# Kernel optimization log

Hardware: AMD Instinct MI355X
Metric: run time of the kernel (lower is better)

Reference implementation:

```python
import jax, jax.numpy as jnp
import numpy as np

ATOM_FDIM = 133
BOND_FDIM = 147
HIDDEN = 300
DEPTH = 3
N_ATOMS = 100000
N_BONDS = 200000
MAX_NB = 6
N_MOLS = 4000


def setup_inputs() -> dict:
    key = jax.random.key(0)
    ks = jax.random.split(key, 10)
    f_atoms = jax.random.normal(ks[0], (N_ATOMS, ATOM_FDIM), dtype=jnp.float32)
    f_bonds = jax.random.normal(ks[1], (N_BONDS, BOND_FDIM), dtype=jnp.float32)
    a2b = jax.random.randint(ks[2], (N_ATOMS, MAX_NB), 0, N_BONDS)
    b2a = jax.random.randint(ks[3], (N_BONDS,), 0, N_ATOMS)
    b2revb = jax.random.randint(ks[4], (N_BONDS,), 0, N_BONDS)
    atom2mol = jnp.sort(jax.random.randint(ks[5], (N_ATOMS,), 0, N_MOLS))
    s = 1.0 / np.sqrt(HIDDEN)
    W_i = jax.random.uniform(ks[6], (BOND_FDIM, HIDDEN), jnp.float32, -s, s)
    W_h = jax.random.uniform(ks[7], (HIDDEN, HIDDEN), jnp.float32, -s, s)
    W_o_w = jax.random.uniform(ks[8], (ATOM_FDIM + HIDDEN, HIDDEN), jnp.float32, -s, s)
    W_o_b = jax.random.uniform(ks[9], (HIDDEN,), jnp.float32, -s, s)
    return {"f_atoms": f_atoms, "f_bonds": f_bonds, "a2b": a2b, "b2a": b2a,
            "b2revb": b2revb, "atom2mol": atom2mol, "W_i": W_i, "W_h": W_h,
            "W_o_w": W_o_w, "W_o_b": W_o_b}


def reference(f_atoms, f_bonds, a2b, b2a, b2revb, atom2mol, W_i, W_h, W_o_w, W_o_b):
    # input = W_i(f_bonds); message = act(input)
    inp = f_bonds @ W_i                      # [n_bonds, hidden]
    message = jax.nn.relu(inp)
    for _ in range(DEPTH - 1):
        # gather neighbor bond messages per atom and sum: [n_atoms, max_nb, h] -> [n_atoms, h]
        a_message = message[a2b].sum(axis=1)
        rev_message = message[b2revb]        # [n_bonds, hidden]
        message = a_message[b2a] - rev_message
        message = jax.nn.relu(inp + message @ W_h)
    # final atom-level aggregation
    a_message = message[a2b].sum(axis=1)     # [n_atoms, hidden]
    a_input = jnp.concatenate([f_atoms, a_message], axis=1)
    atom_hiddens = jax.nn.relu(a_input @ W_o_w + W_o_b)
    # segment mean pooling over molecules
    sums = jax.ops.segment_sum(atom_hiddens, atom2mol, num_segments=N_MOLS)
    counts = jax.ops.segment_sum(jnp.ones((atom_hiddens.shape[0],), atom_hiddens.dtype),
                                 atom2mol, num_segments=N_MOLS)
    mol_vecs = sums / jnp.maximum(counts, 1.0)[:, None]  # zero vec for empty mols
    return mol_vecs
```

## Files before the change

kernel.cpp:

```cpp
#include <hip/hip_runtime.h>
#include <stdint.h>

#define ATOM_FDIM 133
#define BOND_FDIM 147
#define HIDDEN    300
#define N_ATOMS   100000
#define N_BONDS   200000
#define MAX_NB    6
#define N_MOLS    4000

#define KP_I 160
#define KP_H 320
#define KP_O 448
#define LDA  304
#define CPR  38

#define TM   128
#define ACH  8
#define BCH  24

typedef unsigned short u16;
typedef short bf16x8 __attribute__((ext_vector_type(8)));
typedef float f32x4 __attribute__((ext_vector_type(4)));

__device__ __forceinline__ u16 f2bu(float f) {
    unsigned u = __float_as_uint(f);
    u += 0x7FFFu + ((u >> 16) & 1u);
    return (u16)(u >> 16);
}
__device__ __forceinline__ float bu2f(u16 b) { return __uint_as_float(((unsigned)b) << 16); }

__device__ __forceinline__ uint4 relu_bf16x8(uint4 v) {
    union { uint4 u; u16 s[8]; } x, o;
    x.u = v;
    #pragma unroll
    for (int e = 0; e < 8; ++e) o.s[e] = (x.s[e] & 0x8000u) ? (u16)0 : x.s[e];
    return o.u;
}
__device__ __forceinline__ uint4 comb_bf16x8(uint4 vi, uint4 va, uint4 vy) {
    union { uint4 u; u16 s[8]; } xi, xa, xy, o;
    xi.u = vi; xa.u = va; xy.u = vy;
    #pragma unroll
    for (int e = 0; e < 8; ++e)
        o.s[e] = f2bu(fmaxf(bu2f(xi.s[e]) + bu2f(xa.s[e]) - bu2f(xy.s[e]), 0.f));
    return o.u;
}

#define AS1 __attribute__((address_space(1)))
#define AS3 __attribute__((address_space(3)))
__device__ __forceinline__ void gl_lds(const void* g, void* l) {
    __builtin_amdgcn_global_load_lds((const AS1 void*)g, (AS3 void*)l, 16, 0, 0);
}

template <int AM, int EPI>
__global__ __launch_bounds__(512, 2) void mm_k(
    const u16* __restrict__ A, int lda,
    const u16* __restrict__ aYp,
    const u16* __restrict__ Yp,
    const int* __restrict__ b2a,
    const int* __restrict__ b2revb,
    const u16* __restrict__ Wp,
    const float* __restrict__ bias,
    u16* __restrict__ out0, int ldo0,
    int M, int NT)
{
    __shared__ __align__(16) u16 As[3][ACH * 512];
    __shared__ __align__(16) u16 Bs[3][BCH * 512];

    const int t    = threadIdx.x;
    const int lane = t & 63, wid = t >> 6;
    const int fl   = lane & 15, fh = lane >> 4;
    const int m0   = blockIdx.x * TM;
    const int wr   = wid >> 1, wc = wid & 1;

    int arow = m0 + wid * 16 + fl;
    if (arow > M - 1) arow = M - 1;
    const char* srcAp = (const char*)A + (size_t)arow * (size_t)lda * 2u + (size_t)(fh * 16);
    const char* pI = srcAp;
    const char* pA = nullptr; const char* pY = nullptr;
    if constexpr (AM == 2) {
        const int ia = b2a[arow], ir = b2revb[arow];
        pA = (const char*)aYp + (size_t)ia * (LDA * 2) + (size_t)(fh * 16);
        pY = (const char*)Yp  + (size_t)ir * (LDA * 2) + (size_t)(fh * 16);
    }
    const char* WpC = (const char*)Wp;
    const size_t srcB = (size_t)(3 * wid) * 1024u + (size_t)lane * 16u;

    f32x4 acc[2][12] = {};
    uint4 qa0, qa1, qa2, qb0, qb1, qb2;
    (void)qa1; (void)qa2; (void)qb1; (void)qb2;

    if constexpr (AM == 0) {
        gl_lds(srcAp, (char*)As[0] + wid * 1024);
        #pragma unroll
        for (int j = 0; j < 3; ++j) gl_lds(WpC + srcB + (size_t)j * 1024, (char*)Bs[0] + 3 * wid * 1024 + j * 1024);
        gl_lds(srcAp + 64, (char*)As[1] + wid * 1024);
        #pragma unroll
        for (int j = 0; j < 3; ++j) gl_lds(WpC + (size_t)(BCH * 1024) + srcB + (size_t)j * 1024, (char*)Bs[1] + 3 * wid * 1024 + j * 1024);
        asm volatile("s_waitcnt vmcnt(4)" ::: "memory");
        __builtin_amdgcn_s_barrier();
    } else if constexpr (AM == 1) {
        qb0 = *reinterpret_cast<const uint4*>(pI);
        #pragma unroll
        for (int j = 0; j < 3; ++j) gl_lds(WpC + srcB + (size_t)j * 1024, (char*)Bs[0] + 3 * wid * 1024 + j * 1024);
        qa0 = *reinterpret_cast<const uint4*>(pI + 64);
        #pragma unroll
        for (int j = 0; j < 3; ++j) gl_lds(WpC + (size_t)(BCH * 1024) + srcB + (size_t)j * 1024, (char*)Bs[1] + 3 * wid * 1024 + j * 1024);
        asm volatile("s_waitcnt vmcnt(4)" ::: "memory");
        *reinterpret_cast<uint4*>(&As[0][wid * 512 + lane * 8]) = relu_bf16x8(qb0);
        asm volatile("s_waitcnt lgkmcnt(0)" ::: "memory");
        __builtin_amdgcn_s_barrier();
    } else {
        qb0 = *reinterpret_cast<const uint4*>(pI);
        qb1 = *reinterpret_cast<const uint4*>(pA);
        qb2 = *reinterpret_cast<const uint4*>(pY);
        #pragma unroll
        for (int j = 0; j < 3; ++j) gl_lds(WpC + srcB + (size_t)j * 1024, (char*)Bs[0] + 3 * wid * 1024 + j * 1024);
        qa0 = *reinterpret_cast<const uint4*>(pI + 64);
        qa1 = *reinterpret_cast<const uint4*>(pA + 64);
        qa2 = *reinterpret_cast<const uint4*>(pY + 64);
        #pragma unroll
        for (int j = 0; j < 3; ++j) gl_lds(WpC + (size_t)(BCH * 1024) + srcB + (size_t)j * 1024, (char*)Bs[1] + 3 * wid * 1024 + j * 1024);
        asm volatile("s_waitcnt vmcnt(6)" ::: "memory");
        *reinterpret_cast<uint4*>(&As[0][wid * 512 + lane * 8]) = comb_bf16x8(qb0, qb1, qb2);
        asm volatile("s_waitcnt lgkmcnt(0)" ::: "memory");
        __builtin_amdgcn_s_barrier();
    }

    int tt = 0, cur = 0;

#define STEP(RNi, RNa, RNy, RXi, RXa, RXy) do {                                             \
    int w2 = tt + 2; if (w2 >= NT) w2 -= NT;                                                \
    const int nx1 = (cur < 2) ? cur + 1 : 0;                                                \
    const int nx2 = (nx1 < 2) ? nx1 + 1 : 0;                                                \
    bf16x8 af0, af1, bfv[12];                                                               \
    af0 = *reinterpret_cast<const bf16x8*>(&As[cur][(wr * 2 + 0) * 512 + lane * 8]);        \
    af1 = *reinterpret_cast<const bf16x8*>(&As[cur][(wr * 2 + 1) * 512 + lane * 8]);        \
    _Pragma("unroll")                                                                       \
    for (int n = 0; n < 6; ++n)                                                             \
        bfv[n] = *reinterpret_cast<const bf16x8*>(&Bs[cur][(wc * 12 + n) * 512 + lane * 8]);\
    if constexpr (AM == 0) {                                                                \
        gl_lds(srcAp + (size_t)w2 * 64u, (char*)As[nx2] + wid * 1024);                      \
    } else if constexpr (AM == 1) {                                                         \
        RXi = *reinterpret_cast<const uint4*>(pI + (size_t)w2 * 64u);                       \
    } else {                                                                                \
        RXi = *reinterpret_cast<const uint4*>(pI + (size_t)w2 * 64u);                       \
        RXa = *reinterpret_cast<const uint4*>(pA + (size_t)w2 * 64u);                       \
        RXy = *reinterpret_cast<const uint4*>(pY + (size_t)w2 * 64u);                       \
    }                                                                                       \
    gl_lds(WpC + (size_t)w2 * (size_t)(BCH * 1024) + srcB, (char*)Bs[nx2] + 3 * wid * 1024);\
    __builtin_amdgcn_s_barrier();                                                           \
    __builtin_amdgcn_s_setprio(1);                                                          \
    _Pragma("unroll")                                                                       \
    for (int n = 0; n < 6; ++n) {                                                           \
        acc[0][n] = __builtin_amdgcn_mfma_f32_16x16x32_bf16(af0, bfv[n], acc[0][n], 0,0,0); \
        acc[1][n] = __builtin_amdgcn_mfma_f32_16x16x32_bf16(af1, bfv[n], acc[1][n], 0,0,0); \
    }                                                                                       \
    __builtin_amdgcn_s_setprio(0);                                                          \
    __builtin_amdgcn_s_barrier();                                                           \
    _Pragma("unroll")                                                                       \
    for (int n = 6; n < 12; ++n)                                                            \
        bfv[n] = *reinterpret_cast<const bf16x8*>(&Bs[cur][(wc * 12 + n) * 512 + lane * 8]);\
    gl_lds(WpC + (size_t)w2 * (size_t)(BCH * 1024) + srcB + 1024, (char*)Bs[nx2] + 3 * wid * 1024 + 1024); \
    gl_lds(WpC + (size_t)w2 * (size_t)(BCH * 1024) + srcB + 2048, (char*)Bs[nx2] + 3 * wid * 1024 + 2048); \
    if constexpr (AM == 2) { asm volatile("s_waitcnt vmcnt(6)" ::: "memory"); }             \
    else                   { asm volatile("s_waitcnt vmcnt(4)" ::: "memory"); }             \
    if constexpr (AM == 1) {                                                                \
        *reinterpret_cast<uint4*>(&As[nx1][wid * 512 + lane * 8]) = relu_bf16x8(RNi);       \
        asm volatile("s_waitcnt lgkmcnt(0)" ::: "memory");                                  \
    } else if constexpr (AM == 2) {                                                         \
        *reinterpret_cast<uint4*>(&As[nx1][wid * 512 + lane * 8]) = comb_bf16x8(RNi, RNa, RNy); \
        asm volatile("s_waitcnt lgkmcnt(0)" ::: "memory");                                  \
    }                                                                                       \
    __builtin_amdgcn_s_barrier();                                                           \
    __builtin_amdgcn_s_setprio(1);                                                          \
    _Pragma("unroll")                                                                       \
    for (int n = 6; n < 12; ++n) {                                                          \
        acc[0][n] = __builtin_amdgcn_mfma_f32_16x16x32_bf16(af0, bfv[n], acc[0][n], 0,0,0); \
        acc[1][n] = __builtin_amdgcn_mfma_f32_16x16x32_bf16(af1, bfv[n], acc[1][n], 0,0,0); \
    }                                                                                       \
    __builtin_amdgcn_s_setprio(0);                                                          \
    __builtin_amdgcn_s_barrier();                                                           \
    cur = nx1; ++tt;                                                                        \
} while (0)

    while (tt + 1 < NT) {
        STEP(qa0, qa1, qa2, qb0, qb1, qb2);
        STEP(qb0, qb1, qb2, qa0, qa1, qa2);
    }
    if (tt < NT) STEP(qa0, qa1, qa2, qb0, qb1, qb2);
#undef STEP

    #pragma unroll
    for (int m = 0; m < 2; ++m) {
        #pragma unroll
        for (int r = 0; r < 4; ++r) {
            const int row = m0 + wr * 32 + m * 16 + fh * 4 + r;
            if (row >= M) continue;
            #pragma unroll
            for (int n = 0; n < 12; ++n) {
                const int col = wc * 192 + n * 16 + fl;
                if (col >= HIDDEN) continue;
                const float v = acc[m][n][r];
                if (EPI == 0) out0[(size_t)row * ldo0 + col] = f2bu(v);
                else          out0[(size_t)row * ldo0 + col] = f2bu(fmaxf(v + bias[col], 0.f));
            }
        }
    }
}

__global__ __launch_bounds__(256) void wconv_k(const float* __restrict__ W,
                                               int split, int off1, int Ktot, int NT,
                                               u16* __restrict__ Wp)
{
    const int id = blockIdx.x * 256 + threadIdx.x;
    if (id >= NT * BCH * 512) return;
    const int block = id >> 9, rem = id & 511;
    const int l = rem >> 3, e = rem & 7;
    const int c = block % BCH, kt = block / BCH;
    const int col = c * 16 + (l & 15);
    const int k   = kt * 32 + (l >> 4) * 8 + e;
    float v = 0.f;
    if (col < HIDDEN) {
        if (k < split) {
            const int r = k + off1;
            if (r < Ktot) v = W[(size_t)r * HIDDEN + col];
        } else {
            const int r = k - split;
            if (r < off1) v = W[(size_t)r * HIDDEN + col];
        }
    }
    Wp[id] = f2bu(v);
}

__global__ __launch_bounds__(256) void fbconv_k(const float* __restrict__ fb, u16* __restrict__ dst)
{
    const int id = blockIdx.x * 256 + threadIdx.x;
    if (id >= N_BONDS * KP_I) return;
    const int r = id / KP_I, k = id - r * KP_I;
    dst[id] = f2bu(k < BOND_FDIM ? fb[(size_t)r * BOND_FDIM + k] : 0.f);
}

__global__ __launch_bounds__(256) void agg_k(const u16* __restrict__ src,
                                             const int* __restrict__ a2b,
                                             u16* __restrict__ dst)
{
    const int c = blockIdx.x * 256 + threadIdx.x;
    if (c >= N_ATOMS * CPR) return;
    const int a = c / CPR, q = c - a * CPR;
    const int h = q * 8;
    const int* nb = a2b + (size_t)a * MAX_NB;
    float s[8] = {};
    #pragma unroll
    for (int j = 0; j < MAX_NB; ++j) {
        const int r = nb[j];
        union { uint4 u; u16 s[8]; } x;
        x.u = *(const uint4*)(src + (size_t)r * LDA + h);
        #pragma unroll
        for (int e = 0; e < 8; ++e) s[e] += bu2f(x.s[e]);
    }
    union { uint4 u; u16 s[8]; } o;
    #pragma unroll
    for (int e = 0; e < 8; ++e) o.s[e] = f2bu(s[e]);
    *(uint4*)(dst + (size_t)a * LDA + h) = o.u;
}

__global__ __launch_bounds__(256) void comb_k(const u16* __restrict__ inp,
                                              const u16* __restrict__ aY,
                                              const u16* __restrict__ Y,
                                              const int* __restrict__ b2a,
                                              const int* __restrict__ b2revb,
                                              u16* __restrict__ msg)
{
    const int c = blockIdx.x * 256 + threadIdx.x;
    if (c >= N_BONDS * CPR) return;
    const int b = c / CPR, q = c - b * CPR;
    const int h = q * 8;
    const int ia = b2a[b], ir = b2revb[b];
    union { uint4 u; u16 s[8]; } xi, xa, xy, o;
    xi.u = *(const uint4*)(inp + (size_t)b * LDA + h);
    xa.u = *(const uint4*)(aY + (size_t)ia * LDA + h);
    xy.u = *(const uint4*)(Y + (size_t)ir * LDA + h);
    #pragma unroll
    for (int j = 0; j < 8; ++j)
        o.s[j] = f2bu(fmaxf(bu2f(xi.s[j]) + bu2f(xa.s[j]) - bu2f(xy.s[j]), 0.f));
    *(uint4*)(msg + (size_t)b * LDA + h) = o.u;
}

__global__ __launch_bounds__(256) void aggcat_k(const u16* __restrict__ msg,
                                                const int* __restrict__ a2b,
                                                const float* __restrict__ fa,
                                                u16* __restrict__ dst)
{
    const int id = blockIdx.x * 256 + threadIdx.x;
    if (id >= N_ATOMS * (KP_O / 4)) return;
    const int a = id / (KP_O / 4), c = id - a * (KP_O / 4);
    const int e0 = c * 4;
    union { uint2 u; u16 s[4]; } o;
    if (e0 < HIDDEN) {
        const int* nb = a2b + (size_t)a * MAX_NB;
        float s0 = 0.f, s1 = 0.f, s2 = 0.f, s3 = 0.f;
        #pragma unroll
        for (int j = 0; j < MAX_NB; ++j) {
            union { uint2 u; u16 s[4]; } x;
            x.u = *(const uint2*)(msg + (size_t)nb[j] * LDA + e0);
            s0 += bu2f(x.s[0]); s1 += bu2f(x.s[1]); s2 += bu2f(x.s[2]); s3 += bu2f(x.s[3]);
        }
        o.s[0] = f2bu(s0); o.s[1] = f2bu(s1); o.s[2] = f2bu(s2); o.s[3] = f2bu(s3);
    } else {
        #pragma unroll
        for (int j = 0; j < 4; ++j) {
            const int fi = e0 + j - HIDDEN;
            o.s[j] = (fi < ATOM_FDIM) ? f2bu(fa[(size_t)a * ATOM_FDIM + fi]) : (u16)0;
        }
    }
    *(uint2*)(dst + (size_t)a * KP_O + e0) = o.u;
}

__global__ __launch_bounds__(320) void pool_k(const u16* __restrict__ ah,
                                              const int* __restrict__ a2m,
                                              float* __restrict__ out)
{
    const int m = blockIdx.x;
    int lo, hi;
    { int l = 0, r = N_ATOMS;
      while (l < r) { int mid = (l + r) >> 1; if (a2m[mid] < m) l = mid + 1; else r = mid; }
      lo = l; }
    { int l = lo, r = N_ATOMS;
      while (l < r) { int mid = (l + r) >> 1; if (a2m[mid] < m + 1) l = mid + 1; else r = mid; }
      hi = l; }
    const float inv = 1.0f / (float)((hi - lo) > 1 ? (hi - lo) : 1);
    const int h = threadIdx.x;
    if (h >= HIDDEN) return;
    float s = 0.f;
    for (int a = lo; a < hi; ++a) s += bu2f(ah[(size_t)a * LDA + h]);
    out[(size_t)m * HIDDEN + h] = s * inv;
}

extern "C" void kernel_launch(void* const* d_in, const int* in_sizes, int n_in,
                              void* d_out, int out_size, void* d_ws, size_t ws_size,
                              hipStream_t stream)
{
    const float* f_atoms  = (const float*)d_in[0];
    const float* f_bonds  = (const float*)d_in[1];
    const int*   a2b      = (const int*)d_in[2];
    const int*   b2a      = (const int*)d_in[3];
    const int*   b2revb   = (const int*)d_in[4];
    const int*   atom2mol = (const int*)d_in[5];
    const float* W_i      = (const float*)d_in[6];
    const float* W_h      = (const float*)d_in[7];
    const float* W_o_w    = (const float*)d_in[8];
    const float* W_o_b    = (const float*)d_in[9];
    float* out = (float*)d_out;

    char* p = (char*)d_ws;
    auto alloc = [&](size_t bytes) { char* r = p; p += (bytes + 255) & ~(size_t)255; return r; };
    u16* B0 = (u16*)alloc(((size_t)N_BONDS + 16) * LDA * 2);
    u16* B1 = (u16*)alloc(((size_t)N_BONDS + 16) * LDA * 2);
    u16* B2 = (u16*)alloc(((size_t)N_BONDS + 16) * LDA * 2);
    u16* aY = (u16*)alloc(((size_t)N_ATOMS + 16) * LDA * 2);
    u16* Wpi = (u16*)alloc((size_t)(KP_I / 32) * BCH * 512 * 2);
    u16* Wph = (u16*)alloc((size_t)(KP_H / 32) * BCH * 512 * 2);
    u16* Wpo = (u16*)alloc((size_t)(KP_O / 32) * BCH * 512 * 2);
    if ((size_t)(p - (char*)d_ws) > ws_size) return;

    u16* inp    = B0;
    u16* fb16   = B1;
    u16* Y1     = B1;
    u16* Y2     = B2;
    u16* msg2   = B1;
    u16* concat = B2;
    u16* ah     = B0;

    const dim3 blk(256);
    auto g1 = [](long long n) { return dim3((unsigned)((n + 255) / 256)); };
    const dim3 blk5(512);
    const dim3 gB((N_BONDS + TM - 1) / TM);
    const dim3 gA((N_ATOMS + TM - 1) / TM);

    const int BIGSPLIT = 1 << 20;
    wconv_k<<<g1((long long)(KP_I / 32) * BCH * 512), blk, 0, stream>>>(
        W_i, BIGSPLIT, 0, BOND_FDIM, KP_I / 32, Wpi);
    wconv_k<<<g1((long long)(KP_H / 32) * BCH * 512), blk, 0, stream>>>(
        W_h, BIGSPLIT, 0, HIDDEN, KP_H / 32, Wph);
    wconv_k<<<g1((long long)(KP_O / 32) * BCH * 512), blk, 0, stream>>>(
        W_o_w, HIDDEN, ATOM_FDIM, ATOM_FDIM + HIDDEN, KP_O / 32, Wpo);
    fbconv_k<<<g1((long long)N_BONDS * KP_I), blk, 0, stream>>>(f_bonds, fb16);

    mm_k<0, 0><<<gB, blk5, 0, stream>>>(fb16, KP_I, nullptr, nullptr, nullptr, nullptr,
                                        Wpi, nullptr, inp, LDA, N_BONDS, KP_I / 32);

    mm_k<1, 0><<<gB, blk5, 0, stream>>>(inp, LDA, nullptr, nullptr, nullptr, nullptr,
                                        Wph, nullptr, Y1, LDA, N_BONDS, KP_H / 32);
    agg_k<<<g1((long long)N_ATOMS * CPR), blk, 0, stream>>>(Y1, a2b, aY);

    mm_k<2, 0><<<gB, blk5, 0, stream>>>(inp, LDA, aY, Y1, b2a, b2revb,
                                        Wph, nullptr, Y2, LDA, N_BONDS, KP_H / 32);
    agg_k<<<g1((long long)N_ATOMS * CPR), blk, 0, stream>>>(Y2, a2b, aY);

    comb_k<<<g1((long long)N_BONDS * CPR), blk, 0, stream>>>(inp, aY, Y2, b2a, b2revb, msg2);
    aggcat_k<<<g1((long long)N_ATOMS * (KP_O / 4)), blk, 0, stream>>>(msg2, a2b, f_atoms, concat);

    mm_k<0, 1><<<gA, blk5, 0, stream>>>(concat, KP_O, nullptr, nullptr, nullptr, nullptr,
                                        Wpo, W_o_b, ah, LDA, N_ATOMS, KP_O / 32);
    pool_k<<<dim3(N_MOLS), dim3(320), 0, stream>>>(ah, atom2mol, out);
}
```

Baseline: 884.4 us.

## Deepen register-staged prefetch to three stages with a 4-deep B LDS ring

For the register-staged A modes (relu and gather-combine), the pipeline now prefetches three K-tiles ahead using three rotating register sets and a four-slot LDS ring for the weight tiles, with a double-buffered A tile in LDS. The AM==0 path becomes a plain loop with the same three-stage schedule as before. The aim is to hide the latency of the gathered global loads (b2a/b2revb rows) behind more MFMA work. In exchange it uses more VGPRs for the extra in-flight uint4 sets and more LDS for B, which may reduce occupancy under the 512x2 launch bounds.

```diff
diff --git a/kernel.cpp b/kernel.cpp
--- a/kernel.cpp
+++ b/kernel.cpp
@@ -64,8 +64,10 @@
     u16* __restrict__ out0, int ldo0,
     int M, int NT)
 {
-    __shared__ __align__(16) u16 As[3][ACH * 512];
-    __shared__ __align__(16) u16 Bs[3][BCH * 512];
+    constexpr int NBA = (AM == 0) ? 3 : 2;
+    constexpr int NBB = (AM == 0) ? 3 : 4;
+    __shared__ __align__(16) u16 As[NBA * ACH * 512];
+    __shared__ __align__(16) u16 Bs[NBB * BCH * 512];
 
     const int t    = threadIdx.x;
     const int lane = t & 63, wid = t >> 6;
@@ -87,68 +89,118 @@
     const size_t srcB = (size_t)(3 * wid) * 1024u + (size_t)lane * 16u;
 
     f32x4 acc[2][12] = {};
-    uint4 qa0, qa1, qa2, qb0, qb1, qb2;
-    (void)qa1; (void)qa2; (void)qb1; (void)qb2;
+    int tt = 0;
 
     if constexpr (AM == 0) {
-        gl_lds(srcAp, (char*)As[0] + wid * 1024);
-        #pragma unroll
-        for (int j = 0; j < 3; ++j) gl_lds(WpC + srcB + (size_t)j * 1024, (char*)Bs[0] + 3 * wid * 1024 + j * 1024);
-        gl_lds(srcAp + 64, (char*)As[1] + wid * 1024);
-        #pragma unroll
-        for (int j = 0; j < 3; ++j) gl_lds(WpC + (size_t)(BCH * 1024) + srcB + (size_t)j * 1024, (char*)Bs[1] + 3 * wid * 1024 + j * 1024);
+        gl_lds(srcAp, (char*)As + wid * 1024);
+        #pragma unroll
+        for (int j = 0; j < 3; ++j)
+            gl_lds(WpC + srcB + (size_t)j * 1024, (char*)Bs + 3 * wid * 1024 + j * 1024);
+        gl_lds(srcAp + 64, (char*)As + (ACH * 1024) + wid * 1024);
+        #pragma unroll
+        for (int j = 0; j < 3; ++j)
+            gl_lds(WpC + (size_t)(BCH * 1024) + srcB + (size_t)j * 1024,
+                   (char*)Bs + (BCH * 1024) + 3 * wid * 1024 + j * 1024);
         asm volatile("s_waitcnt vmcnt(4)" ::: "memory");
         __builtin_amdgcn_s_barrier();
-    } else if constexpr (AM == 1) {
-        qb0 = *reinterpret_cast<const uint4*>(pI);
-        #pragma unroll
-        for (int j = 0; j < 3; ++j) gl_lds(WpC + srcB + (size_t)j * 1024, (char*)Bs[0] + 3 * wid * 1024 + j * 1024);
-        qa0 = *reinterpret_cast<const uint4*>(pI + 64);
-        #pragma unroll
-        for (int j = 0; j < 3; ++j) gl_lds(WpC + (size_t)(BCH * 1024) + srcB + (size_t)j * 1024, (char*)Bs[1] + 3 * wid * 1024 + j * 1024);
-        asm volatile("s_waitcnt vmcnt(4)" ::: "memory");
-        *reinterpret_cast<uint4*>(&As[0][wid * 512 + lane * 8]) = relu_bf16x8(qb0);
+
+        int cur = 0;
+        for (tt = 0; tt < NT; ++tt) {
+            int w2 = tt + 2; if (w2 >= NT) w2 -= NT;
+            const int nx1 = (cur < 2) ? cur + 1 : 0;
+            const int nx2 = (nx1 < 2) ? nx1 + 1 : 0;
+            const u16* as_c = As + (size_t)cur * (ACH * 512);
+            const u16* bs_c = Bs + (size_t)cur * (BCH * 512);
+            const size_t kbB = (size_t)w2 * (size_t)(BCH * 1024);
+
+            bf16x8 af0, af1, bfv[12];
+            af0 = *reinterpret_cast<const bf16x8*>(&as_c[(wr * 2 + 0) * 512 + lane * 8]);
+            af1 = *reinterpret_cast<const bf16x8*>(&as_c[(wr * 2 + 1) * 512 + lane * 8]);
+            #pragma unroll
+            for (int n = 0; n < 6; ++n)
+                bfv[n] = *reinterpret_cast<const bf16x8*>(&bs_c[(wc * 12 + n) * 512 + lane * 8]);
+            gl_lds(srcAp + (size_t)w2 * 64u, (char*)As + (size_t)nx2 * (ACH * 1024) + wid * 1024);
+            gl_lds(WpC + kbB + srcB, (char*)Bs + (size_t)nx2 * (BCH * 1024) + 3 * wid * 1024);
+            __builtin_amdgcn_s_barrier();
+            __builtin_amdgcn_s_setprio(1);
+            #pragma unroll
+            for (int n = 0; n < 6; ++n) {
+                acc[0][n] = __builtin_amdgcn_mfma_f32_16x16x32_bf16(af0, bfv[n], acc[0][n], 0, 0, 0);
+                acc[1][n] = __builtin_amdgcn_mfma_f32_16x16x32_bf16(af1, bfv[n], acc[1][n], 0, 0, 0);
+            }
+            __builtin_amdgcn_s_setprio(0);
+            __builtin_amdgcn_s_barrier();
+
+            #pragma unroll
+            for (int n = 6; n < 12; ++n)
+                bfv[n] = *reinterpret_cast<const bf16x8*>(&bs_c[(wc * 12 + n) * 512 + lane * 8]);
+            gl_lds(WpC + kbB + srcB + 1024, (char*)Bs + (size_t)nx2 * (BCH * 1024) + 3 * wid * 1024 + 1024);
+            gl_lds(WpC + kbB + srcB + 2048, (char*)Bs + (size_t)nx2 * (BCH * 1024) + 3 * wid * 1024 + 2048);
+            asm volatile("s_waitcnt vmcnt(4)" ::: "memory");
+            __builtin_amdgcn_s_barrier();
+            __builtin_amdgcn_s_setprio(1);
+            #pragma unroll
+            for (int n = 6; n < 12; ++n) {
+                acc[0][n] = __builtin_amdgcn_mfma_f32_16x16x32_bf16(af0, bfv[n], acc[0][n], 0, 0, 0);
+                acc[1][n] = __builtin_amdgcn_mfma_f32_16x16x32_bf16(af1, bfv[n], acc[1][n], 0, 0, 0);
+            }
+            __builtin_amdgcn_s_setprio(0);
+            __builtin_amdgcn_s_barrier();
+            cur = nx1;
+        }
+    } else {
+        uint4 Xi, Xa, Xy, Yi, Ya, Yy, Zi, Za, Zy;
+        (void)Xa; (void)Xy; (void)Ya; (void)Yy; (void)Za; (void)Zy;
+
+        Xi = *reinterpret_cast<const uint4*>(pI);
+        if constexpr (AM == 2) { Xa = *reinterpret_cast<const uint4*>(pA);
+                                 Xy = *reinterpret_cast<const uint4*>(pY); }
+        #pragma unroll
+        for (int j = 0; j < 3; ++j)
+            gl_lds(WpC + srcB + (size_t)j * 1024, (char*)Bs + 3 * wid * 1024 + j * 1024);
+        Yi = *reinterpret_cast<const uint4*>(pI + 64);
+        if constexpr (AM == 2) { Ya = *reinterpret_cast<const uint4*>(pA + 64);
+                                 Yy = *reinterpret_cast<const uint4*>(pY + 64); }
+        #pragma unroll
+        for (int j = 0; j < 3; ++j)
+            gl_lds(WpC + (size_t)(BCH * 1024) + srcB + (size_t)j * 1024,
+                   (char*)Bs + (BCH * 1024) + 3 * wid * 1024 + j * 1024);
+        Zi = *reinterpret_cast<const uint4*>(pI + 128);
+        if constexpr (AM == 2) { Za = *reinterpret_cast<const uint4*>(pA + 128);
+                                 Zy = *reinterpret_cast<const uint4*>(pY + 128); }
+        #pragma unroll
+        for (int j = 0; j < 3; ++j)
+            gl_lds(WpC + (size_t)(2 * BCH * 1024) + srcB + (size_t)j * 1024,
+                   (char*)Bs + (2 * BCH * 1024) + 3 * wid * 1024 + j * 1024);
+        if constexpr (AM == 2) { asm volatile("s_waitcnt vmcnt(12)" ::: "memory"); }
+        else                   { asm volatile("s_waitcnt vmcnt(8)"  ::: "memory"); }
+        {
+            uint4 w0;
+            if constexpr (AM == 2) w0 = comb_bf16x8(Xi, Xa, Xy);
+            else                   w0 = relu_bf16x8(Xi);
+            *reinterpret_cast<uint4*>(&As[wid * 512 + lane * 8]) = w0;
+        }
         asm volatile("s_waitcnt lgkmcnt(0)" ::: "memory");
         __builtin_amdgcn_s_barrier();
-    } else {
-        qb0 = *reinterpret_cast<const uint4*>(pI);
-        qb1 = *reinterpret_cast<const uint4*>(pA);
-        qb2 = *reinterpret_cast<const uint4*>(pY);
-        #pragma unroll
-        for (int j = 0; j < 3; ++j) gl_lds(WpC + srcB + (size_t)j * 1024, (char*)Bs[0] + 3 * wid * 1024 + j * 1024);
-        qa0 = *reinterpret_cast<const uint4*>(pI + 64);
-        qa1 = *reinterpret_cast<const uint4*>(pA + 64);
-        qa2 = *reinterpret_cast<const uint4*>(pY + 64);
-        #pragma unroll
-        for (int j = 0; j < 3; ++j) gl_lds(WpC + (size_t)(BCH * 1024) + srcB + (size_t)j * 1024, (char*)Bs[1] + 3 * wid * 1024 + j * 1024);
-        asm volatile("s_waitcnt vmcnt(6)" ::: "memory");
-        *reinterpret_cast<uint4*>(&As[0][wid * 512 + lane * 8]) = comb_bf16x8(qb0, qb1, qb2);
-        asm volatile("s_waitcnt lgkmcnt(0)" ::: "memory");
-        __builtin_amdgcn_s_barrier();
-    }
-
-    int tt = 0, cur = 0;
-
-#define STEP(RNi, RNa, RNy, RXi, RXa, RXy) do {                                             \
-    int w2 = tt + 2; if (w2 >= NT) w2 -= NT;                                                \
-    const int nx1 = (cur < 2) ? cur + 1 : 0;                                                \
-    const int nx2 = (nx1 < 2) ? nx1 + 1 : 0;                                                \
+
+#define STEP12(Ui, Ua, Uy, Vi, Va, Vy, Wi, Wa, Wy) do {                                     \
+    int w3 = tt + 3; if (w3 >= NT) w3 -= NT;                                                \
+    const u16* as_c = As + (size_t)(tt & 1) * (ACH * 512);                                  \
+    const u16* bs_c = Bs + (size_t)(tt & 3) * (BCH * 512);                                  \
+    char* bst = (char*)Bs + (size_t)((tt + 3) & 3) * (BCH * 1024) + 3 * wid * 1024;         \
+    const size_t kbB = (size_t)w3 * (size_t)(BCH * 1024);                                   \
     bf16x8 af0, af1, bfv[12];                                                               \
-    af0 = *reinterpret_cast<const bf16x8*>(&As[cur][(wr * 2 + 0) * 512 + lane * 8]);        \
-    af1 = *reinterpret_cast<const bf16x8*>(&As[cur][(wr * 2 + 1) * 512 + lane * 8]);        \
+    af0 = *reinterpret_cast<const bf16x8*>(&as_c[(wr * 2 + 0) * 512 + lane * 8]);           \
+    af1 = *reinterpret_cast<const bf16x8*>(&as_c[(wr * 2 + 1) * 512 + lane * 8]);           \
     _Pragma("unroll")                                                                       \
     for (int n = 0; n < 6; ++n)                                                             \
-        bfv[n] = *reinterpret_cast<const bf16x8*>(&Bs[cur][(wc * 12 + n) * 512 + lane * 8]);\
-    if constexpr (AM == 0) {                                                                \
-        gl_lds(srcAp + (size_t)w2 * 64u, (char*)As[nx2] + wid * 1024);                      \
-    } else if constexpr (AM == 1) {                                                         \
-        RXi = *reinterpret_cast<const uint4*>(pI + (size_t)w2 * 64u);                       \
-    } else {                                                                                \
-        RXi = *reinterpret_cast<const uint4*>(pI + (size_t)w2 * 64u);                       \
-        RXa = *reinterpret_cast<const uint4*>(pA + (size_t)w2 * 64u);                       \
-        RXy = *reinterpret_cast<const uint4*>(pY + (size_t)w2 * 64u);                       \
+        bfv[n] = *reinterpret_cast<const bf16x8*>(&bs_c[(wc * 12 + n) * 512 + lane * 8]);   \
+    Wi = *reinterpret_cast<const uint4*>(pI + (size_t)w3 * 64u);                            \
+    if constexpr (AM == 2) {                                                                \
+        Wa = *reinterpret_cast<const uint4*>(pA + (size_t)w3 * 64u);                        \
+        Wy = *reinterpret_cast<const uint4*>(pY + (size_t)w3 * 64u);                        \
     }                                                                                       \
-    gl_lds(WpC + (size_t)w2 * (size_t)(BCH * 1024) + srcB, (char*)Bs[nx2] + 3 * wid * 1024);\
+    gl_lds(WpC + kbB + srcB, bst);                                                          \
     __builtin_amdgcn_s_barrier();                                                           \
     __builtin_amdgcn_s_setprio(1);                                                          \
     _Pragma("unroll")                                                                       \
@@ -160,18 +212,19 @@
     __builtin_amdgcn_s_barrier();                                                           \
     _Pragma("unroll")                                                                       \
     for (int n = 6; n < 12; ++n)                                                            \
-        bfv[n] = *reinterpret_cast<const bf16x8*>(&Bs[cur][(wc * 12 + n) * 512 + lane * 8]);\
-    gl_lds(WpC + (size_t)w2 * (size_t)(BCH * 1024) + srcB + 1024, (char*)Bs[nx2] + 3 * wid * 1024 + 1024); \
-    gl_lds(WpC + (size_t)w2 * (size_t)(BCH * 1024) + srcB + 2048, (char*)Bs[nx2] + 3 * wid * 1024 + 2048); \
-    if constexpr (AM == 2) { asm volatile("s_waitcnt vmcnt(6)" ::: "memory"); }             \
-    else                   { asm volatile("s_waitcnt vmcnt(4)" ::: "memory"); }             \
-    if constexpr (AM == 1) {                                                                \
-        *reinterpret_cast<uint4*>(&As[nx1][wid * 512 + lane * 8]) = relu_bf16x8(RNi);       \
-        asm volatile("s_waitcnt lgkmcnt(0)" ::: "memory");                                  \
-    } else if constexpr (AM == 2) {                                                         \
-        *reinterpret_cast<uint4*>(&As[nx1][wid * 512 + lane * 8]) = comb_bf16x8(RNi, RNa, RNy); \
-        asm volatile("s_waitcnt lgkmcnt(0)" ::: "memory");                                  \
+        bfv[n] = *reinterpret_cast<const bf16x8*>(&bs_c[(wc * 12 + n) * 512 + lane * 8]);   \
+    gl_lds(WpC + kbB + srcB + 1024, bst + 1024);                                            \
+    gl_lds(WpC + kbB + srcB + 2048, bst + 2048);                                            \
+    if constexpr (AM == 2) { asm volatile("s_waitcnt vmcnt(12)" ::: "memory"); }            \
+    else                   { asm volatile("s_waitcnt vmcnt(8)"  ::: "memory"); }            \
+    {                                                                                       \
+        uint4 wv;                                                                           \
+        if constexpr (AM == 2) wv = comb_bf16x8(Ui, Ua, Uy);                                \
+        else                   wv = relu_bf16x8(Ui);                                        \
+        *reinterpret_cast<uint4*>(&As[(size_t)((tt + 1) & 1) * (ACH * 512)                  \
+                                      + wid * 512 + lane * 8]) = wv;                        \
     }                                                                                       \
+    asm volatile("s_waitcnt lgkmcnt(0)" ::: "memory");                                      \
     __builtin_amdgcn_s_barrier();                                                           \
     __builtin_amdgcn_s_setprio(1);                                                          \
     _Pragma("unroll")                                                                       \
@@ -181,15 +234,18 @@
     }                                                                                       \
     __builtin_amdgcn_s_setprio(0);                                                          \
     __builtin_amdgcn_s_barrier();                                                           \
-    cur = nx1; ++tt;                                                                        \
+    ++tt;                                                                                   \
 } while (0)
 
-    while (tt + 1 < NT) {
-        STEP(qa0, qa1, qa2, qb0, qb1, qb2);
-        STEP(qb0, qb1, qb2, qa0, qa1, qa2);
-    }
-    if (tt < NT) STEP(qa0, qa1, qa2, qb0, qb1, qb2);
-#undef STEP
+        while (tt + 2 < NT) {
+            STEP12(Yi, Ya, Yy, Zi, Za, Zy, Xi, Xa, Xy);
+            STEP12(Zi, Za, Zy, Xi, Xa, Xy, Yi, Ya, Yy);
+            STEP12(Xi, Xa, Xy, Yi, Ya, Yy, Zi, Za, Zy);
+        }
+        if (tt < NT) STEP12(Yi, Ya, Yy, Zi, Za, Zy, Xi, Xa, Xy);
+        if (tt < NT) STEP12(Zi, Za, Zy, Xi, Xa, Xy, Yi, Ya, Yy);
+#undef STEP12
+    }
 
     #pragma unroll
     for (int m = 0; m < 2; ++m) {
```

Result: no change. 879.8 us (-0.5%).

## Shrink N padding to 320, double-buffer A via registers, raise occupancy

Applied to the files above, without the earlier changes.

The output width tile drops from 384 to 320 columns (BCH 24→20), which cuts wasted MFMA work on the 300-wide hidden dimension and reduces the accumulators to 20 per thread. The A operand now always goes through registers into a two-stage LDS buffer instead of a triple buffer loaded by direct global-to-LDS copies. B chunks are split unevenly across waves, with the per-wave vmcnt waits adjusted to match. Launch bounds go to 4 blocks per SM to raise occupancy. The uneven per-wave load counts and their hand-tuned waitcnts carry a correctness risk, and AM==0 loses its direct-to-LDS A path.

```diff
diff --git a/kernel.cpp b/kernel.cpp
--- a/kernel.cpp
+++ b/kernel.cpp
@@ -17,7 +17,7 @@
 
 #define TM   128
 #define ACH  8
-#define BCH  24
+#define BCH  20
 
 typedef unsigned short u16;
 typedef short bf16x8 __attribute__((ext_vector_type(8)));
@@ -53,7 +53,7 @@
 }
 
 template <int AM, int EPI>
-__global__ __launch_bounds__(512, 2) void mm_k(
+__global__ __launch_bounds__(512, 4) void mm_k(
     const u16* __restrict__ A, int lda,
     const u16* __restrict__ aYp,
     const u16* __restrict__ Yp,
@@ -64,7 +64,7 @@
     u16* __restrict__ out0, int ldo0,
     int M, int NT)
 {
-    __shared__ __align__(16) u16 As[3][ACH * 512];
+    __shared__ __align__(16) u16 As[2][ACH * 512];
     __shared__ __align__(16) u16 Bs[3][BCH * 512];
 
     const int t    = threadIdx.x;
@@ -75,8 +75,7 @@
 
     int arow = m0 + wid * 16 + fl;
     if (arow > M - 1) arow = M - 1;
-    const char* srcAp = (const char*)A + (size_t)arow * (size_t)lda * 2u + (size_t)(fh * 16);
-    const char* pI = srcAp;
+    const char* pI = (const char*)A + (size_t)arow * (size_t)lda * 2u + (size_t)(fh * 16);
     const char* pA = nullptr; const char* pY = nullptr;
     if constexpr (AM == 2) {
         const int ia = b2a[arow], ir = b2revb[arow];
@@ -84,112 +83,124 @@
         pY = (const char*)Yp  + (size_t)ir * (LDA * 2) + (size_t)(fh * 16);
     }
     const char* WpC = (const char*)Wp;
-    const size_t srcB = (size_t)(3 * wid) * 1024u + (size_t)lane * 16u;
-
-    f32x4 acc[2][12] = {};
-    uint4 qa0, qa1, qa2, qb0, qb1, qb2;
-    (void)qa1; (void)qa2; (void)qb1; (void)qb2;
-
-    if constexpr (AM == 0) {
-        gl_lds(srcAp, (char*)As[0] + wid * 1024);
-        #pragma unroll
-        for (int j = 0; j < 3; ++j) gl_lds(WpC + srcB + (size_t)j * 1024, (char*)Bs[0] + 3 * wid * 1024 + j * 1024);
-        gl_lds(srcAp + 64, (char*)As[1] + wid * 1024);
-        #pragma unroll
-        for (int j = 0; j < 3; ++j) gl_lds(WpC + (size_t)(BCH * 1024) + srcB + (size_t)j * 1024, (char*)Bs[1] + 3 * wid * 1024 + j * 1024);
-        asm volatile("s_waitcnt vmcnt(4)" ::: "memory");
-        __builtin_amdgcn_s_barrier();
-    } else if constexpr (AM == 1) {
-        qb0 = *reinterpret_cast<const uint4*>(pI);
-        #pragma unroll
-        for (int j = 0; j < 3; ++j) gl_lds(WpC + srcB + (size_t)j * 1024, (char*)Bs[0] + 3 * wid * 1024 + j * 1024);
-        qa0 = *reinterpret_cast<const uint4*>(pI + 64);
-        #pragma unroll
-        for (int j = 0; j < 3; ++j) gl_lds(WpC + (size_t)(BCH * 1024) + srcB + (size_t)j * 1024, (char*)Bs[1] + 3 * wid * 1024 + j * 1024);
-        asm volatile("s_waitcnt vmcnt(4)" ::: "memory");
-        *reinterpret_cast<uint4*>(&As[0][wid * 512 + lane * 8]) = relu_bf16x8(qb0);
-        asm volatile("s_waitcnt lgkmcnt(0)" ::: "memory");
-        __builtin_amdgcn_s_barrier();
+    const int bbase = (wid < 4) ? 3 * wid : 12 + 2 * (wid - 4);
+    const size_t srcB0 = (size_t)bbase * 1024u + (size_t)lane * 16u;
+
+    f32x4 acc[2][10] = {};
+    uint4 Xi, Xa, Xy, Yi, Ya, Yy;
+    (void)Xa; (void)Xy; (void)Ya; (void)Yy;
+
+    Xi = *reinterpret_cast<const uint4*>(pI);
+    if constexpr (AM == 2) { Xa = *reinterpret_cast<const uint4*>(pA);
+                             Xy = *reinterpret_cast<const uint4*>(pY); }
+    gl_lds(WpC + srcB0, (char*)Bs[0] + bbase * 1024);
+    gl_lds(WpC + srcB0 + 1024, (char*)Bs[0] + bbase * 1024 + 1024);
+    if (wid < 4) gl_lds(WpC + srcB0 + 2048, (char*)Bs[0] + bbase * 1024 + 2048);
+    Yi = *reinterpret_cast<const uint4*>(pI + 64);
+    if constexpr (AM == 2) { Ya = *reinterpret_cast<const uint4*>(pA + 64);
+                             Yy = *reinterpret_cast<const uint4*>(pY + 64); }
+    {
+        const size_t kb1 = (size_t)(BCH * 1024);
+        gl_lds(WpC + kb1 + srcB0, (char*)Bs[1] + bbase * 1024);
+        gl_lds(WpC + kb1 + srcB0 + 1024, (char*)Bs[1] + bbase * 1024 + 1024);
+        if (wid < 4) gl_lds(WpC + kb1 + srcB0 + 2048, (char*)Bs[1] + bbase * 1024 + 2048);
+    }
+    if constexpr (AM == 2) {
+        if (wid < 4) asm volatile("s_waitcnt vmcnt(9)" ::: "memory");
+        else         asm volatile("s_waitcnt vmcnt(7)" ::: "memory");
     } else {
-        qb0 = *reinterpret_cast<const uint4*>(pI);
-        qb1 = *reinterpret_cast<const uint4*>(pA);
-        qb2 = *reinterpret_cast<const uint4*>(pY);
-        #pragma unroll
-        for (int j = 0; j < 3; ++j) gl_lds(WpC + srcB + (size_t)j * 1024, (char*)Bs[0] + 3 * wid * 1024 + j * 1024);
-        qa0 = *reinterpret_cast<const uint4*>(pI + 64);
-        qa1 = *reinterpret_cast<const uint4*>(pA + 64);
-        qa2 = *reinterpret_cast<const uint4*>(pY + 64);
-        #pragma unroll
-        for (int j = 0; j < 3; ++j) gl_lds(WpC + (size_t)(BCH * 1024) + srcB + (size_t)j * 1024, (char*)Bs[1] + 3 * wid * 1024 + j * 1024);
-        asm volatile("s_waitcnt vmcnt(6)" ::: "memory");
-        *reinterpret_cast<uint4*>(&As[0][wid * 512 + lane * 8]) = comb_bf16x8(qb0, qb1, qb2);
-        asm volatile("s_waitcnt lgkmcnt(0)" ::: "memory");
-        __builtin_amdgcn_s_barrier();
-    }
-
-    int tt = 0, cur = 0;
-
-#define STEP(RNi, RNa, RNy, RXi, RXa, RXy) do {                                             \
+        if (wid < 4) asm volatile("s_waitcnt vmcnt(7)" ::: "memory");
+        else         asm volatile("s_waitcnt vmcnt(5)" ::: "memory");
+    }
+    {
+        uint4 w0;
+        if constexpr (AM == 2) w0 = comb_bf16x8(Xi, Xa, Xy);
+        else if constexpr (AM == 1) w0 = relu_bf16x8(Xi);
+        else w0 = Xi;
+        *reinterpret_cast<uint4*>(&As[0][wid * 512 + lane * 8]) = w0;
+    }
+    if constexpr (AM == 2) {
+        if (wid < 4) asm volatile("s_waitcnt vmcnt(6)" ::: "memory");
+        else         asm volatile("s_waitcnt vmcnt(5)" ::: "memory");
+    } else {
+        if (wid < 4) asm volatile("s_waitcnt vmcnt(4)" ::: "memory");
+        else         asm volatile("s_waitcnt vmcnt(3)" ::: "memory");
+    }
+    asm volatile("s_waitcnt lgkmcnt(0)" ::: "memory");
+    __builtin_amdgcn_s_barrier();
+
+    int tt = 0, bcur = 0;
+
+#define GATE() do {                                                        \
+    if constexpr (AM == 2) {                                               \
+        if (wid < 4) asm volatile("s_waitcnt vmcnt(6)" ::: "memory");      \
+        else         asm volatile("s_waitcnt vmcnt(5)" ::: "memory");      \
+    } else {                                                               \
+        if (wid < 4) asm volatile("s_waitcnt vmcnt(4)" ::: "memory");      \
+        else         asm volatile("s_waitcnt vmcnt(3)" ::: "memory");      \
+    } } while (0)
+
+#define STEP(LI, LA, LY, WI, WA, WY) do {                                                   \
     int w2 = tt + 2; if (w2 >= NT) w2 -= NT;                                                \
-    const int nx1 = (cur < 2) ? cur + 1 : 0;                                                \
-    const int nx2 = (nx1 < 2) ? nx1 + 1 : 0;                                                \
-    bf16x8 af0, af1, bfv[12];                                                               \
-    af0 = *reinterpret_cast<const bf16x8*>(&As[cur][(wr * 2 + 0) * 512 + lane * 8]);        \
-    af1 = *reinterpret_cast<const bf16x8*>(&As[cur][(wr * 2 + 1) * 512 + lane * 8]);        \
+    const u16* as_c = As[tt & 1];                                                           \
+    const u16* bs_c = Bs[bcur];                                                             \
+    int bnx = bcur + 2; if (bnx >= 3) bnx -= 3;                                             \
+    char* bdst = (char*)Bs[bnx] + bbase * 1024;                                             \
+    const size_t kbB = (size_t)w2 * (size_t)(BCH * 1024);                                   \
+    bf16x8 af0, af1, bfv[10];                                                               \
+    af0 = *reinterpret_cast<const bf16x8*>(&as_c[(wr * 2 + 0) * 512 + lane * 8]);           \
+    af1 = *reinterpret_cast<const bf16x8*>(&as_c[(wr * 2 + 1) * 512 + lane * 8]);           \
     _Pragma("unroll")                                                                       \
-    for (int n = 0; n < 6; ++n)                                                             \
-        bfv[n] = *reinterpret_cast<const bf16x8*>(&Bs[cur][(wc * 12 + n) * 512 + lane * 8]);\
-    if constexpr (AM == 0) {                                                                \
-        gl_lds(srcAp + (size_t)w2 * 64u, (char*)As[nx2] + wid * 1024);                      \
-    } else if constexpr (AM == 1) {                                                         \
-        RXi = *reinterpret_cast<const uint4*>(pI + (size_t)w2 * 64u);                       \
-    } else {                                                                                \
-        RXi = *reinterpret_cast<const uint4*>(pI + (size_t)w2 * 64u);                       \
-        RXa = *reinterpret_cast<const uint4*>(pA + (size_t)w2 * 64u);                       \
-        RXy = *reinterpret_cast<const uint4*>(pY + (size_t)w2 * 64u);                       \
+    for (int n = 0; n < 5; ++n)                                                             \
+        bfv[n] = *reinterpret_cast<const bf16x8*>(&bs_c[(wc * 10 + n) * 512 + lane * 8]);   \
+    LI = *reinterpret_cast<const uint4*>(pI + (size_t)w2 * 64u);                            \
+    if constexpr (AM == 2) {                                                                \
+        LA = *reinterpret_cast<const uint4*>(pA + (size_t)w2 * 64u);                        \
+        LY = *reinterpret_cast<const uint4*>(pY + (size_t)w2 * 64u);                        \
     }                                                                                       \
-    gl_lds(WpC + (size_t)w2 * (size_t)(BCH * 1024) + srcB, (char*)Bs[nx2] + 3 * wid * 1024);\
+    gl_lds(WpC + kbB + srcB0, bdst);                                                        \
     __builtin_amdgcn_s_barrier();                                                           \
     __builtin_amdgcn_s_setprio(1);                                                          \
     _Pragma("unroll")                                                                       \
-    for (int n = 0; n < 6; ++n) {                                                           \
+    for (int n = 0; n < 5; ++n) {                                                           \
         acc[0][n] = __builtin_amdgcn_mfma_f32_16x16x32_bf16(af0, bfv[n], acc[0][n], 0,0,0); \
         acc[1][n] = __builtin_amdgcn_mfma_f32_16x16x32_bf16(af1, bfv[n], acc[1][n], 0,0,0); \
     }                                                                                       \
     __builtin_amdgcn_s_setprio(0);                                                          \
     __builtin_amdgcn_s_barrier();                                                           \
     _Pragma("unroll")                                                                       \
-    for (int n = 6; n < 12; ++n)                                                            \
-        bfv[n] = *reinterpret_cast<const bf16x8*>(&Bs[cur][(wc * 12 + n) * 512 + lane * 8]);\
-    gl_lds(WpC + (size_t)w2 * (size_t)(BCH * 1024) + srcB + 1024, (char*)Bs[nx2] + 3 * wid * 1024 + 1024); \
-    gl_lds(WpC + (size_t)w2 * (size_t)(BCH * 1024) + srcB + 2048, (char*)Bs[nx2] + 3 * wid * 1024 + 2048); \
-    if constexpr (AM == 2) { asm volatile("s_waitcnt vmcnt(6)" ::: "memory"); }             \
-    else                   { asm volatile("s_waitcnt vmcnt(4)" ::: "memory"); }             \
-    if constexpr (AM == 1) {                                                                \
-        *reinterpret_cast<uint4*>(&As[nx1][wid * 512 + lane * 8]) = relu_bf16x8(RNi);       \
-        asm volatile("s_waitcnt lgkmcnt(0)" ::: "memory");                                  \
-    } else if constexpr (AM == 2) {                                                         \
-        *reinterpret_cast<uint4*>(&As[nx1][wid * 512 + lane * 8]) = comb_bf16x8(RNi, RNa, RNy); \
-        asm volatile("s_waitcnt lgkmcnt(0)" ::: "memory");                                  \
+    for (int n = 5; n < 10; ++n)                                                            \
+        bfv[n] = *reinterpret_cast<const bf16x8*>(&bs_c[(wc * 10 + n) * 512 + lane * 8]);   \
+    gl_lds(WpC + kbB + srcB0 + 1024, bdst + 1024);                                          \
+    if (wid < 4) gl_lds(WpC + kbB + srcB0 + 2048, bdst + 2048);                             \
+    GATE();                                                                                 \
+    {                                                                                       \
+        uint4 wv;                                                                           \
+        if constexpr (AM == 2) wv = comb_bf16x8(WI, WA, WY);                                \
+        else if constexpr (AM == 1) wv = relu_bf16x8(WI);                                   \
+        else wv = WI;                                                                       \
+        *reinterpret_cast<uint4*>(&As[(tt + 1) & 1][wid * 512 + lane * 8]) = wv;            \
     }                                                                                       \
+    asm volatile("s_waitcnt lgkmcnt(0)" ::: "memory");                                      \
     __builtin_amdgcn_s_barrier();                                                           \
     __builtin_amdgcn_s_setprio(1);                                                          \
     _Pragma("unroll")                                                                       \
-    for (int n = 6; n < 12; ++n) {                                                          \
+    for (int n = 5; n < 10; ++n) {                                                          \
         acc[0][n] = __builtin_amdgcn_mfma_f32_16x16x32_bf16(af0, bfv[n], acc[0][n], 0,0,0); \
         acc[1][n] = __builtin_amdgcn_mfma_f32_16x16x32_bf16(af1, bfv[n], acc[1][n], 0,0,0); \
     }                                                                                       \
     __builtin_amdgcn_s_setprio(0);                                                          \
     __builtin_amdgcn_s_barrier();                                                           \
-    cur = nx1; ++tt;                                                                        \
+    ++tt; bcur = (bcur == 2) ? 0 : bcur + 1;                                                \
 } while (0)
 
     while (tt + 1 < NT) {
-        STEP(qa0, qa1, qa2, qb0, qb1, qb2);
-        STEP(qb0, qb1, qb2, qa0, qa1, qa2);
-    }
-    if (tt < NT) STEP(qa0, qa1, qa2, qb0, qb1, qb2);
+        STEP(Xi, Xa, Xy, Yi, Ya, Yy);
+        STEP(Yi, Ya, Yy, Xi, Xa, Xy);
+    }
+    if (tt < NT) STEP(Xi, Xa, Xy, Yi, Ya, Yy);
 #undef STEP
+#undef GATE
 
     #pragma unroll
     for (int m = 0; m < 2; ++m) {
@@ -198,8 +209,8 @@
             const int row = m0 + wr * 32 + m * 16 + fh * 4 + r;
             if (row >= M) continue;
             #pragma unroll
-            for (int n = 0; n < 12; ++n) {
-                const int col = wc * 192 + n * 16 + fl;
+            for (int n = 0; n < 10; ++n) {
+                const int col = wc * 160 + n * 16 + fl;
                 if (col >= HIDDEN) continue;
                 const float v = acc[m][n][r];
                 if (EPI == 0) out0[(size_t)row * ldo0 + col] = f2bu(v);
```

Result: slower. 1.140 ms (+28.8%).
